# Performance work log

Measured on AMD Instinct MI355X. Metric: run time of the kernel, lower is better.

Reference implementation:

```python
import jax, jax.numpy as jnp
import numpy as np

B, N, R, T, E, H, FE = 2, 512, 64, 128, 64, 8, 4
D = E // H  # head_dim = 8


def _layernorm(x, g, b):
    m = x.mean(-1, keepdims=True)
    v = ((x - m) ** 2).mean(-1, keepdims=True)
    return (x - m) / jnp.sqrt(v + 1e-5) * g + b


def _sattn(v, k, q, Wv, Wk, Wq, Wo, bo, mask):
    # v,k: (Bk,Nk,T,E); q: (Bq,Nq,T,E) with Bq possibly 1 (broadcast on batch)
    Bk, Nk, Tk, _ = v.shape
    Nq = q.shape[1]
    v = v.reshape(Bk, Nk, Tk, H, D) @ Wv
    k = k.reshape(Bk, Nk, Tk, H, D) @ Wk
    q = q.reshape(q.shape[0], Nq, Tk, H, D) @ Wq
    q = jnp.broadcast_to(q, (Bk, Nq, Tk, H, D))
    energy = jnp.einsum('bqthd,bkthd->bqkth', q, k)  # (B,Nq,Nk,T,H)
    if mask is not None:
        m = mask[None, :, :, None, None]
        energy = energy * m + (-1e8) * (1.0 - m)
    # note: non-standard softmax over the QUERY axis (dim=1), after scale+clamp
    att = jax.nn.softmax(jnp.clip(energy * (float(E) ** -0.5), -5.0, 5.0), axis=1)
    out = jnp.einsum('bqkth,bkthd->bqthd', att, v).reshape(Bk, Nq, Tk, E)
    return out @ Wo + bo, att


def setup_inputs() -> dict:
    rng = jax.random.key(0)
    ks = jax.random.split(rng, 40)
    s = 0.05
    inp = {
        'value': jax.random.normal(ks[0], (B, N, T, E), jnp.float32),
        'key': jax.random.normal(ks[1], (B, N, T, E), jnp.float32),
        'query': jax.random.normal(ks[2], (B, N, T, E), jnp.float32),
        'adj_sr': jax.random.randint(ks[3], (N, R), 0, 2).astype(jnp.int32),
        'adj_r': jax.random.randint(ks[4], (R, R), 0, 2).astype(jnp.int32),
        'D_S': jax.random.normal(ks[5], (N, R), jnp.float32) * s,
        'W_emb': jax.random.normal(ks[6], (R, E), jnp.float32) * s,
        'b_emb': jnp.zeros((E,), jnp.float32),
        'I_param': jax.random.normal(ks[7], (R, 1, E), jnp.float32) * s,
        'g1': jnp.ones((E,), jnp.float32), 'beta1': jnp.zeros((E,), jnp.float32),
        'g2': jnp.ones((E,), jnp.float32), 'beta2': jnp.zeros((E,), jnp.float32),
        'W_ff1': jax.random.normal(ks[8], (E, FE * E), jnp.float32) * s,
        'b_ff1': jnp.zeros((FE * E,), jnp.float32),
        'W_ff2': jax.random.normal(ks[9], (FE * E, E), jnp.float32) * s,
        'b_ff2': jnp.zeros((E,), jnp.float32),
        'W_fs': jax.random.normal(ks[10], (E, E), jnp.float32) * s,
        'b_fs': jnp.zeros((E,), jnp.float32),
    }
    i = 11
    for tag in ('sr', 'rr', 'rs'):
        inp['Wv_' + tag] = jax.random.normal(ks[i + 0], (D, D), jnp.float32) * s
        inp['Wk_' + tag] = jax.random.normal(ks[i + 1], (D, D), jnp.float32) * s
        inp['Wq_' + tag] = jax.random.normal(ks[i + 2], (D, D), jnp.float32) * s
        inp['Wo_' + tag] = jax.random.normal(ks[i + 3], (E, E), jnp.float32) * s
        inp['bo_' + tag] = jnp.zeros((E,), jnp.float32)
        i += 4
    return inp


def reference(value, key, query, adj_sr, adj_r, D_S, W_emb, b_emb, I_param,
              g1, beta1, g2, beta2, W_ff1, b_ff1, W_ff2, b_ff2, W_fs, b_fs,
              Wv_sr, Wk_sr, Wq_sr, Wo_sr, bo_sr,
              Wv_rr, Wk_rr, Wq_rr, Wo_rr, bo_rr,
              Wv_rs, Wk_rs, Wq_rs, Wo_rs, bo_rs):
    m_sr = adj_sr.T.astype(jnp.float32)  # (R,N)
    m_r = adj_r.astype(jnp.float32)      # (R,R)
    ds = D_S @ W_emb + b_emb             # (N,E)
    q = query + ds[None, :, None, :]
    k = key + ds[None, :, None, :]
    v = value
    Iq = jnp.broadcast_to(I_param[None], (1, R, T, E))  # I.repeat(1,1,T,1)
    Hh, asr = _sattn(v, k, Iq, Wv_sr, Wk_sr, Wq_sr, Wo_sr, bo_sr, m_sr)
    Hh, arr = _sattn(Hh, Hh, Hh, Wv_rr, Wk_rr, Wq_rr, Wo_rr, bo_rr, m_r)
    attn, ars = _sattn(Hh, Hh, q, Wv_rs, Wk_rs, Wq_rs, Wo_rs, bo_rs, None)
    x = _layernorm(attn + q, g1, beta1)          # dropout=0.0 -> identity
    ff = jax.nn.relu(x @ W_ff1 + b_ff1) @ W_ff2 + b_ff2
    U = _layernorm(ff + x, g2, beta2)
    out = U @ W_fs + b_fs
    return (out, asr, arr, ars, Hh)
```

## Files before the change

### kernel.cpp

```cpp
#include <hip/hip_runtime.h>
#include <hip/hip_bf16.h>

typedef __hip_bfloat16 bf16;

#define Bc 2
#define Nc 512
#define Rc 64
#define Tc 128
#define Ec 64
#define Hc 8
#define THc 1024
#define FFc 256

__device__ __forceinline__ bf16  f2b(float x){ return __float2bfloat16(x); }
__device__ __forceinline__ float us2f(unsigned short u){
  union { unsigned int i; float f; } c; c.i = ((unsigned int)u) << 16; return c.f;
}
__device__ __forceinline__ float clip5(float x){ return fminf(fmaxf(x, -5.0f), 5.0f); }

__device__ __forceinline__ float wave_sum64(float v){
#pragma unroll
  for (int o = 32; o > 0; o >>= 1) v += __shfl_xor(v, o, 64);
  return v;
}
__device__ __forceinline__ void wave_sum64x2(float& a, float& b){
#pragma unroll
  for (int o = 32; o > 0; o >>= 1){
    a += __shfl_xor(a, o, 64);
    b += __shfl_xor(b, o, 64);
  }
}

__device__ __forceinline__ float rowred16_sum(float v){
  v += __shfl_xor(v, 1, 64);
  v += __shfl_xor(v, 2, 64);
  v += __shfl_xor(v, 4, 64);
  v += __shfl_xor(v, 8, 64);
  return v;
}

__global__ __launch_bounds__(64) void k_prep(
    const float* __restrict__ DS, const float* __restrict__ Wemb,
    const float* __restrict__ bemb, const float* __restrict__ Ip,
    const float* __restrict__ Wq, float* __restrict__ ds, float* __restrict__ qhat)
{
  int bid = blockIdx.x, t = threadIdx.x;
  if (bid < Nc){
    int n = bid, e = t;
    __shared__ float row[Rc];
    row[t] = DS[n*Rc + t];
    __syncthreads();
    float acc = bemb[e];
    for (int r = 0; r < Rc; ++r) acc += row[r] * Wemb[r*Ec + e];
    ds[n*Ec + e] = acc;
  } else {
    int r = bid - Nc;
    __shared__ float irow[Ec];
    irow[t] = Ip[r*Ec + t];
    __syncthreads();
    int h = t >> 3, d = t & 7;
    float acc = 0.0f;
#pragma unroll
    for (int d0 = 0; d0 < 8; ++d0) acc += irow[h*8 + d0] * Wq[d0*8 + d];
    qhat[r*Ec + h*8 + d] = acc;
  }
}

__global__ __launch_bounds__(256) void k_proj_sr(
    const float* __restrict__ key, const float* __restrict__ value,
    const float* __restrict__ ds, const float* __restrict__ Wk,
    const float* __restrict__ Wv, float* __restrict__ khat, float* __restrict__ vhat)
{
  __shared__ float wk[64], wv[64];
  int t = threadIdx.x;
  if (t < 64){ wk[t] = Wk[t]; wv[t] = Wv[t]; }
  __syncthreads();
  int u = blockIdx.x*256 + t;
  int h = u & 7;
  int nt = u >> 3;
  int n = (nt / Tc) % Nc;
  const float* kp = key + (size_t)u*8;
  const float* vp = value + (size_t)u*8;
  const float* dsp = ds + n*Ec + h*8;
  float kin[8], vin[8];
#pragma unroll
  for (int d = 0; d < 8; ++d){ kin[d] = kp[d] + dsp[d]; vin[d] = vp[d]; }
  float* ko = khat + (size_t)u*8;
  float* vo = vhat + (size_t)u*8;
#pragma unroll
  for (int d = 0; d < 8; ++d){
    float ka = 0.0f, va = 0.0f;
#pragma unroll
    for (int d0 = 0; d0 < 8; ++d0){ ka += kin[d0]*wk[d0*8+d]; va += vin[d0]*wv[d0*8+d]; }
    ko[d] = ka; vo[d] = va;
  }
}

__global__ __launch_bounds__(256) void k_attn_sr(
    const float* __restrict__ khat, const float* __restrict__ vhat,
    const float* __restrict__ qhat, const int* __restrict__ adj_sr,
    bf16* __restrict__ att_c, float* __restrict__ pre)
{
  __shared__ float accs[4][64][8];
  int bid = blockIdx.x;
  int b = bid >> 10, th = bid & 1023;
  int t = th >> 3, h = th & 7;
  int tid = threadIdx.x;
  int r = tid & 63, w = tid >> 6;
  float q[8];
#pragma unroll
  for (int d = 0; d < 8; ++d) q[d] = qhat[r*Ec + h*8 + d];
  float acc[8] = {0,0,0,0,0,0,0,0};
  int n0 = w*128;
  for (int n = n0; n < n0 + 128; n += 2){
    size_t goA = ((size_t)((b*Nc + n)*Tc + t))*Ec + h*8;
    size_t goB = goA + (size_t)Tc*Ec;
    const float* kA = khat + goA;
    const float* kB = khat + goB;
    float eA = 0.0f, eB = 0.0f;
#pragma unroll
    for (int d = 0; d < 8; ++d){ eA += q[d]*kA[d]; eB += q[d]*kB[d]; }
    int mA = adj_sr[n*Rc + r], mB = adj_sr[(n+1)*Rc + r];
    eA = mA ? clip5(eA*0.125f) : -5.0f;
    eB = mB ? clip5(eB*0.125f) : -5.0f;
    float pA = __expf(eA), pB = __expf(eB);
    float sA = pA, sB = pB;
    wave_sum64x2(sA, sB);
    float aA = pA/sA, aB = pB/sB;
    size_t ao = ((size_t)(b*Nc + n)*THc + th)*Rc + r;
    att_c[ao] = f2b(aA);
    att_c[ao + (size_t)THc*Rc] = f2b(aB);
    const float* vA = vhat + goA;
    const float* vB = vhat + goB;
#pragma unroll
    for (int d = 0; d < 8; ++d) acc[d] += aA*vA[d] + aB*vB[d];
  }
#pragma unroll
  for (int d = 0; d < 8; ++d) accs[w][r][d] = acc[d];
  __syncthreads();
  if (w == 0){
    size_t po = ((size_t)((b*Rc + r)*Tc + t))*Ec + h*8;
#pragma unroll
    for (int d = 0; d < 8; ++d)
      pre[po + d] = accs[0][r][d] + accs[1][r][d] + accs[2][r][d] + accs[3][r][d];
  }
}

__global__ __launch_bounds__(256) void k_attn_rr(
    const float* __restrict__ qh, const float* __restrict__ kh,
    const float* __restrict__ vh, const int* __restrict__ adj_r,
    bf16* __restrict__ att_c, float* __restrict__ pre)
{
  __shared__ float accs[4][64][8];
  int bid = blockIdx.x;
  int b = bid >> 10, th = bid & 1023;
  int t = th >> 3, h = th & 7;
  int tid = threadIdx.x;
  int q = tid & 63, w = tid >> 6;
  size_t qo = ((size_t)((b*Rc + q)*Tc + t))*Ec + h*8;
  float qv[8];
#pragma unroll
  for (int d = 0; d < 8; ++d) qv[d] = qh[qo + d];
  float acc[8] = {0,0,0,0,0,0,0,0};
  int k0 = w*16;
  for (int k = k0; k < k0 + 16; k += 2){
    size_t koA = ((size_t)((b*Rc + k)*Tc + t))*Ec + h*8;
    size_t koB = koA + (size_t)Tc*Ec;
    const float* kA = kh + koA;
    const float* kB = kh + koB;
    float eA = 0.0f, eB = 0.0f;
#pragma unroll
    for (int d = 0; d < 8; ++d){ eA += qv[d]*kA[d]; eB += qv[d]*kB[d]; }
    int mA = adj_r[q*Rc + k], mB = adj_r[q*Rc + k + 1];
    eA = mA ? clip5(eA*0.125f) : -5.0f;
    eB = mB ? clip5(eB*0.125f) : -5.0f;
    float pA = __expf(eA), pB = __expf(eB);
    float sA = pA, sB = pB;
    wave_sum64x2(sA, sB);
    float aA = pA/sA, aB = pB/sB;
    size_t ao = ((size_t)(b*Rc + k)*THc + th)*Rc + q;
    att_c[ao] = f2b(aA);
    att_c[ao + (size_t)THc*Rc] = f2b(aB);
    const float* vA = vh + koA;
    const float* vB = vh + koB;
#pragma unroll
    for (int d = 0; d < 8; ++d) acc[d] += aA*vA[d] + aB*vB[d];
  }
#pragma unroll
  for (int d = 0; d < 8; ++d) accs[w][q][d] = acc[d];
  __syncthreads();
  if (w == 0){
#pragma unroll
    for (int d = 0; d < 8; ++d)
      pre[qo + d] = accs[0][q][d] + accs[1][q][d] + accs[2][q][d] + accs[3][q][d];
  }
}

__global__ __launch_bounds__(512) void k_attn_rs(
    const float* __restrict__ query, const float* __restrict__ ds,
    const float* __restrict__ Wq, const float* __restrict__ kh,
    const float* __restrict__ vh, bf16* __restrict__ att_c, float* __restrict__ pre)
{
  __shared__ float wq[64];
  __shared__ float kl[64][8];
  __shared__ float vl[64][8];
  __shared__ float redS[2][2][8];
  int bid = blockIdx.x;
  int b = bid >> 10, th = bid & 1023;
  int t = th >> 3, h = th & 7;
  int q = threadIdx.x;
  if (q < 64) wq[q] = Wq[q];
  {
    int kk = q >> 3, d = q & 7;
    size_t o = ((size_t)((b*Rc + kk)*Tc + t))*Ec + h*8 + d;
    kl[kk][d] = kh[o];
    vl[kk][d] = vh[o];
  }
  __syncthreads();
  size_t qro = ((size_t)((b*Nc + q)*Tc + t))*Ec + h*8;
  const float* dsp = ds + q*Ec + h*8;
  float xin[8], qv[8];
#pragma unroll
  for (int d = 0; d < 8; ++d) xin[d] = query[qro + d] + dsp[d];
#pragma unroll
  for (int d = 0; d < 8; ++d){
    float a = 0.0f;
#pragma unroll
    for (int d0 = 0; d0 < 8; ++d0) a += xin[d0]*wq[d0*8 + d];
    qv[d] = a;
  }
  float acc[8] = {0,0,0,0,0,0,0,0};
  int lane = q & 63, wv = q >> 6;
  for (int k = 0; k < 64; k += 2){
    float eA = 0.0f, eB = 0.0f;
#pragma unroll
    for (int d = 0; d < 8; ++d){ eA += qv[d]*kl[k][d]; eB += qv[d]*kl[k+1][d]; }
    eA = clip5(eA*0.125f);
    eB = clip5(eB*0.125f);
    float pA = __expf(eA), pB = __expf(eB);
    float sA = pA, sB = pB;
    wave_sum64x2(sA, sB);
    int pb = (k >> 1) & 1;
    if (lane == 0){ redS[pb][0][wv] = sA; redS[pb][1][wv] = sB; }
    __syncthreads();
    float stA = 0.0f, stB = 0.0f;
#pragma unroll
    for (int i = 0; i < 8; ++i){ stA += redS[pb][0][i]; stB += redS[pb][1][i]; }
    float aA = pA/stA, aB = pB/stB;
    size_t ao = ((size_t)(b*Rc + k)*THc + th)*Nc + q;
    att_c[ao] = f2b(aA);
    att_c[ao + (size_t)THc*Nc] = f2b(aB);
#pragma unroll
    for (int d = 0; d < 8; ++d) acc[d] += aA*vl[k][d] + aB*vl[k+1][d];
  }
#pragma unroll
  for (int d = 0; d < 8; ++d) pre[qro + d] = acc[d];
}

__global__ __launch_bounds__(256) void k_transpose(
    const unsigned short* __restrict__ src, float* __restrict__ dst,
    int W, int C)
{
  __shared__ unsigned short tile[64][66];
  int bid = blockIdx.x;
  int nct = C >> 6;
  int ct = bid % nct; bid /= nct;
  int tht = bid & 15; bid >>= 4;
  int w = bid % W; int b = bid / W;
  int tt = threadIdx.x;
  {
    int cs = tt & 63, i0 = tt >> 6;
    const unsigned short* sb = src + ((size_t)(b*W + w)*THc + tht*64)*C + ct*64;
#pragma unroll
    for (int p = 0; p < 16; ++p){
      int i = i0 + p*4;
      tile[i][cs] = sb[(size_t)i*C + cs];
    }
  }
  __syncthreads();
  {
    int i = tt & 63, c0 = tt >> 6;
#pragma unroll
    for (int p = 0; p < 16; ++p){
      int cs = c0 + p*4;
      int c = ct*64 + cs;
      dst[((size_t)(b*C + c)*W + w)*THc + tht*64 + i] = us2f(tile[i][cs]);
    }
  }
}

__global__ __launch_bounds__(256) void k_wo(
    const float* __restrict__ pre, const float* __restrict__ Wo,
    const float* __restrict__ bo, float* __restrict__ outf,
    float* __restrict__ outf2, int nrows)
{
  int gt = blockIdx.x*256 + threadIdx.x;
  int row = gt >> 6, lane = gt & 63;
  if (row >= nrows) return;
  float xin = pre[(size_t)row*64 + lane];
  float acc = bo[lane];
  for (int e = 0; e < 64; ++e){
    float xe = __shfl(xin, e, 64);
    acc += xe * Wo[e*64 + lane];
  }
  outf[(size_t)row*64 + lane] = acc;
  if (outf2) outf2[(size_t)row*64 + lane] = acc;
}

__global__ __launch_bounds__(256) void k_proj3(
    const float* __restrict__ src, const float* Wq, const float* Wk, const float* Wv,
    float* qh, float* kh, float* vh, int nunits)
{
  __shared__ float wq[64], wk[64], wv[64];
  int t = threadIdx.x;
  if (t < 64){
    wq[t] = Wq ? Wq[t] : 0.0f;
    wk[t] = Wk[t];
    wv[t] = Wv[t];
  }
  __syncthreads();
  int u = blockIdx.x*256 + t;
  if (u >= nunits) return;
  const float* sp = src + (size_t)u*8;
  float xin[8];
#pragma unroll
  for (int d = 0; d < 8; ++d) xin[d] = sp[d];
#pragma unroll
  for (int d = 0; d < 8; ++d){
    float qa = 0.0f, ka = 0.0f, va = 0.0f;
#pragma unroll
    for (int d0 = 0; d0 < 8; ++d0){
      qa += xin[d0]*wq[d0*8 + d];
      ka += xin[d0]*wk[d0*8 + d];
      va += xin[d0]*wv[d0*8 + d];
    }
    if (qh) qh[(size_t)u*8 + d] = qa;
    kh[(size_t)u*8 + d] = ka;
    vh[(size_t)u*8 + d] = va;
  }
}

__device__ __forceinline__ void gemm64x64(
    const float (* __restrict__ Xs)[68], const float* __restrict__ W,
    int Wld, int r0, int c0, float acc[4][4])
{
#pragma unroll 4
  for (int k = 0; k < 64; k += 4){
    float4 xr0 = *(const float4*)&Xs[r0+0][k];
    float4 xr1 = *(const float4*)&Xs[r0+1][k];
    float4 xr2 = *(const float4*)&Xs[r0+2][k];
    float4 xr3 = *(const float4*)&Xs[r0+3][k];
#pragma unroll
    for (int kk = 0; kk < 4; ++kk){
      float4 w = *(const float4*)&W[(size_t)(k+kk)*Wld + c0];
      float x0 = (&xr0.x)[kk], x1 = (&xr1.x)[kk];
      float x2 = (&xr2.x)[kk], x3 = (&xr3.x)[kk];
      acc[0][0] += x0*w.x; acc[0][1] += x0*w.y; acc[0][2] += x0*w.z; acc[0][3] += x0*w.w;
      acc[1][0] += x1*w.x; acc[1][1] += x1*w.y; acc[1][2] += x1*w.z; acc[1][3] += x1*w.w;
      acc[2][0] += x2*w.x; acc[2][1] += x2*w.y; acc[2][2] += x2*w.z; acc[2][3] += x2*w.w;
      acc[3][0] += x3*w.x; acc[3][1] += x3*w.y; acc[3][2] += x3*w.z; acc[3][3] += x3*w.w;
    }
  }
}

__device__ __forceinline__ void ln64(
    const float acc[4][4], float4 g, float4 b, float out[4][4])
{
#pragma unroll
  for (int i = 0; i < 4; ++i){
    float s = acc[i][0] + acc[i][1] + acc[i][2] + acc[i][3];
    float m = rowred16_sum(s) * (1.0f/64.0f);
    float d0 = acc[i][0] - m, d1 = acc[i][1] - m, d2 = acc[i][2] - m, d3 = acc[i][3] - m;
    float vv = d0*d0 + d1*d1 + d2*d2 + d3*d3;
    float var = rowred16_sum(vv) * (1.0f/64.0f);
    float rs = rsqrtf(var + 1e-5f);
    out[i][0] = d0*rs*g.x + b.x;
    out[i][1] = d1*rs*g.y + b.y;
    out[i][2] = d2*rs*g.z + b.z;
    out[i][3] = d3*rs*g.w + b.w;
  }
}

__global__ __launch_bounds__(256) void k_tail(
    const float* __restrict__ pre3, const float* __restrict__ query,
    const float* __restrict__ ds,
    const float* __restrict__ Wo, const float* __restrict__ bo,
    const float* __restrict__ g1, const float* __restrict__ be1,
    const float* __restrict__ W1, const float* __restrict__ b1,
    const float* __restrict__ W2, const float* __restrict__ b2,
    const float* __restrict__ g2, const float* __restrict__ be2,
    const float* __restrict__ Wfs, const float* __restrict__ bfs,
    float* __restrict__ outp)
{
  __shared__ float Xs[64][68];
  __shared__ float Hs[64][68];
  int tid = threadIdx.x;
  int cg = tid & 15, rg = tid >> 4;
  int r0 = rg*4, c0 = cg*4;
  int row_base = blockIdx.x * 64;
  int n = (row_base >> 7) & (Nc - 1);

#pragma unroll
  for (int i = 0; i < 4; ++i){
    float4 t = *(const float4*)&pre3[(size_t)(row_base + r0 + i)*64 + c0];
    *(float4*)&Xs[r0+i][c0] = t;
  }

  float4 bo4  = *(const float4*)&bo[c0];
  float4 ds4  = *(const float4*)&ds[n*64 + c0];
  float4 g14  = *(const float4*)&g1[c0];
  float4 be14 = *(const float4*)&be1[c0];
  float4 b24  = *(const float4*)&b2[c0];
  float4 g24  = *(const float4*)&g2[c0];
  float4 be24 = *(const float4*)&be2[c0];
  float4 bfs4 = *(const float4*)&bfs[c0];
  __syncthreads();

  float acc[4][4];
#pragma unroll
  for (int i = 0; i < 4; ++i){
    acc[i][0] = bo4.x; acc[i][1] = bo4.y; acc[i][2] = bo4.z; acc[i][3] = bo4.w;
  }
  gemm64x64(Xs, Wo, 64, r0, c0, acc);
#pragma unroll
  for (int i = 0; i < 4; ++i){
    float4 qv = *(const float4*)&query[(size_t)(row_base + r0 + i)*64 + c0];
    acc[i][0] += qv.x + ds4.x;
    acc[i][1] += qv.y + ds4.y;
    acc[i][2] += qv.z + ds4.z;
    acc[i][3] += qv.w + ds4.w;
  }
  float xt[4][4];
  ln64(acc, g14, be14, xt);
  __syncthreads();
#pragma unroll
  for (int i = 0; i < 4; ++i)
    *(float4*)&Xs[r0+i][c0] = make_float4(xt[i][0], xt[i][1], xt[i][2], xt[i][3]);
  __syncthreads();

  float ff[4][4];
#pragma unroll
  for (int i = 0; i < 4; ++i){
    ff[i][0] = b24.x; ff[i][1] = b24.y; ff[i][2] = b24.z; ff[i][3] = b24.w;
  }
  for (int p = 0; p < 4; ++p){
    float4 b14 = *(const float4*)&b1[p*64 + c0];
    float h[4][4];
#pragma unroll
    for (int i = 0; i < 4; ++i){
      h[i][0] = b14.x; h[i][1] = b14.y; h[i][2] = b14.z; h[i][3] = b14.w;
    }
    gemm64x64(Xs, W1 + p*64, 256, r0, c0, h);
#pragma unroll
    for (int i = 0; i < 4; ++i){
      h[i][0] = fmaxf(h[i][0], 0.0f); h[i][1] = fmaxf(h[i][1], 0.0f);
      h[i][2] = fmaxf(h[i][2], 0.0f); h[i][3] = fmaxf(h[i][3], 0.0f);
    }
    __syncthreads();
#pragma unroll
    for (int i = 0; i < 4; ++i)
      *(float4*)&Hs[r0+i][c0] = make_float4(h[i][0], h[i][1], h[i][2], h[i][3]);
    __syncthreads();
    gemm64x64(Hs, W2 + (size_t)p*64*64, 64, r0, c0, ff);
  }

#pragma unroll
  for (int i = 0; i < 4; ++i){
    float4 xv = *(const float4*)&Xs[r0+i][c0];
    ff[i][0] += xv.x; ff[i][1] += xv.y; ff[i][2] += xv.z; ff[i][3] += xv.w;
  }
  float U[4][4];
  ln64(ff, g24, be24, U);
  __syncthreads();
#pragma unroll
  for (int i = 0; i < 4; ++i)
    *(float4*)&Hs[r0+i][c0] = make_float4(U[i][0], U[i][1], U[i][2], U[i][3]);
  __syncthreads();

  float o[4][4];
#pragma unroll
  for (int i = 0; i < 4; ++i){
    o[i][0] = bfs4.x; o[i][1] = bfs4.y; o[i][2] = bfs4.z; o[i][3] = bfs4.w;
  }
  gemm64x64(Hs, Wfs, 64, r0, c0, o);
#pragma unroll
  for (int i = 0; i < 4; ++i)
    *(float4*)&outp[(size_t)(row_base + r0 + i)*64 + c0] =
        make_float4(o[i][0], o[i][1], o[i][2], o[i][3]);
}

extern "C" void kernel_launch(void* const* d_in, const int* in_sizes, int n_in,
                              void* d_out, int out_size, void* d_ws, size_t ws_size,
                              hipStream_t stream)
{
  const float* value = (const float*)d_in[0];
  const float* key   = (const float*)d_in[1];
  const float* query = (const float*)d_in[2];
  const int*  adj_sr = (const int*)d_in[3];
  const int*  adj_r  = (const int*)d_in[4];
  const float* D_S   = (const float*)d_in[5];
  const float* W_emb = (const float*)d_in[6];
  const float* b_emb = (const float*)d_in[7];
  const float* I_par = (const float*)d_in[8];
  const float* g1    = (const float*)d_in[9];
  const float* be1   = (const float*)d_in[10];
  const float* g2    = (const float*)d_in[11];
  const float* be2   = (const float*)d_in[12];
  const float* W_ff1 = (const float*)d_in[13];
  const float* b_ff1 = (const float*)d_in[14];
  const float* W_ff2 = (const float*)d_in[15];
  const float* b_ff2 = (const float*)d_in[16];
  const float* W_fs  = (const float*)d_in[17];
  const float* b_fs  = (const float*)d_in[18];
  const float* Wv_sr = (const float*)d_in[19];
  const float* Wk_sr = (const float*)d_in[20];
  const float* Wq_sr = (const float*)d_in[21];
  const float* Wo_sr = (const float*)d_in[22];
  const float* bo_sr = (const float*)d_in[23];
  const float* Wv_rr = (const float*)d_in[24];
  const float* Wk_rr = (const float*)d_in[25];
  const float* Wq_rr = (const float*)d_in[26];
  const float* Wo_rr = (const float*)d_in[27];
  const float* bo_rr = (const float*)d_in[28];
  const float* Wv_rs = (const float*)d_in[29];
  const float* Wk_rs = (const float*)d_in[30];
  const float* Wq_rs = (const float*)d_in[31];
  const float* Wo_rs = (const float*)d_in[32];
  const float* bo_rs = (const float*)d_in[33];

  float* outp  = (float*)d_out;
  float* o_out = outp;
  float* o_asr = outp + 8388608;
  float* o_arr = outp + 75497472;
  float* o_ars = outp + 83886080;
  float* o_hh  = outp + 150994944;

  float* wsf = (float*)d_ws;
  float* ws_ds   = wsf;
  float* ws_qsr  = wsf + 32768;
  bf16*  ws_att  = (bf16*)(wsf + 36864);
  float* pool    = wsf + 36864 + 33554432;
  float* ws_ksr  = pool;
  float* ws_vsr  = pool + 8388608;
  float* ws_pre1 = pool + 16777216;
  float* ws_hh1  = pool + 17825792;
  float* ws_qrr  = pool;
  float* ws_krr  = pool + 1048576;
  float* ws_vrr  = pool + 2097152;
  float* ws_pre2 = pool + 3145728;
  float* ws_hh2  = pool + 4194304;
  float* ws_krs  = pool + 5242880;
  float* ws_vrs  = pool + 6291456;
  float* ws_pre3 = pool + 7340032;

  k_prep<<<576, 64, 0, stream>>>(D_S, W_emb, b_emb, I_par, Wq_sr, ws_ds, ws_qsr);
  k_proj_sr<<<4096, 256, 0, stream>>>(key, value, ws_ds, Wk_sr, Wv_sr, ws_ksr, ws_vsr);
  k_attn_sr<<<2048, 256, 0, stream>>>(ws_ksr, ws_vsr, ws_qsr, adj_sr, ws_att, ws_pre1);
  k_transpose<<<16384, 256, 0, stream>>>((const unsigned short*)ws_att, o_asr, 512, 64);
  k_wo<<<4096, 256, 0, stream>>>(ws_pre1, Wo_sr, bo_sr, ws_hh1, (float*)nullptr, 16384);

  k_proj3<<<512, 256, 0, stream>>>(ws_hh1, Wq_rr, Wk_rr, Wv_rr,
                                   ws_qrr, ws_krr, ws_vrr, 131072);
  k_attn_rr<<<2048, 256, 0, stream>>>(ws_qrr, ws_krr, ws_vrr, adj_r, ws_att, ws_pre2);
  k_transpose<<<2048, 256, 0, stream>>>((const unsigned short*)ws_att, o_arr, 64, 64);
  k_wo<<<4096, 256, 0, stream>>>(ws_pre2, Wo_rr, bo_rr, ws_hh2, o_hh, 16384);

  k_proj3<<<512, 256, 0, stream>>>(ws_hh2, (const float*)nullptr, Wk_rs, Wv_rs,
                                   (float*)nullptr, ws_krs, ws_vrs, 131072);
  k_attn_rs<<<2048, 512, 0, stream>>>(query, ws_ds, Wq_rs, ws_krs, ws_vrs,
                                      ws_att, ws_pre3);
  k_transpose<<<16384, 256, 0, stream>>>((const unsigned short*)ws_att, o_ars, 64, 512);

  k_tail<<<2048, 256, 0, stream>>>(ws_pre3, query, ws_ds, Wo_rs, bo_rs,
                                   g1, be1, W_ff1, b_ff1, W_ff2, b_ff2,
                                   g2, be2, W_fs, b_fs, o_out);
}
```

Measured before the change: 848.8 us.

## Process all heads per thread in sr/rr attention and write fp32 attention directly

The sr and rr attention kernels now have each thread handle all 8 heads for one (b,t) with 64-wide register q/acc arrays and vectorized float4 loads. Attention weights are written straight into the final output layout as float4, which removes the bf16 staging buffer and the separate transpose launches. The sr kernel splits N into 4 partial sums that k_wo now adds up. Costs are much higher register pressure, lower occupancy (256 blocks for rr), and a 16-step shared-memory reduction with barriers.

```diff
diff --git a/kernel.cpp b/kernel.cpp
--- a/kernel.cpp
+++ b/kernel.cpp
@@ -99,100 +99,154 @@
 __global__ __launch_bounds__(256) void k_attn_sr(
     const float* __restrict__ khat, const float* __restrict__ vhat,
     const float* __restrict__ qhat, const int* __restrict__ adj_sr,
-    bf16* __restrict__ att_c, float* __restrict__ pre)
-{
-  __shared__ float accs[4][64][8];
+    float* __restrict__ o_asr, float* __restrict__ pre_part)
+{
+  __shared__ float red[2][4][64][4];
   int bid = blockIdx.x;
-  int b = bid >> 10, th = bid & 1023;
-  int t = th >> 3, h = th & 7;
+  int nh = bid & 3; int bt = bid >> 2;
+  int t = bt & (Tc - 1); int b = bt >> 7;
   int tid = threadIdx.x;
   int r = tid & 63, w = tid >> 6;
-  float q[8];
-#pragma unroll
-  for (int d = 0; d < 8; ++d) q[d] = qhat[r*Ec + h*8 + d];
-  float acc[8] = {0,0,0,0,0,0,0,0};
-  int n0 = w*128;
-  for (int n = n0; n < n0 + 128; n += 2){
-    size_t goA = ((size_t)((b*Nc + n)*Tc + t))*Ec + h*8;
-    size_t goB = goA + (size_t)Tc*Ec;
-    const float* kA = khat + goA;
-    const float* kB = khat + goB;
-    float eA = 0.0f, eB = 0.0f;
-#pragma unroll
-    for (int d = 0; d < 8; ++d){ eA += q[d]*kA[d]; eB += q[d]*kB[d]; }
-    int mA = adj_sr[n*Rc + r], mB = adj_sr[(n+1)*Rc + r];
-    eA = mA ? clip5(eA*0.125f) : -5.0f;
-    eB = mB ? clip5(eB*0.125f) : -5.0f;
-    float pA = __expf(eA), pB = __expf(eB);
-    float sA = pA, sB = pB;
-    wave_sum64x2(sA, sB);
-    float aA = pA/sA, aB = pB/sB;
-    size_t ao = ((size_t)(b*Nc + n)*THc + th)*Rc + r;
-    att_c[ao] = f2b(aA);
-    att_c[ao + (size_t)THc*Rc] = f2b(aB);
-    const float* vA = vhat + goA;
-    const float* vB = vhat + goB;
-#pragma unroll
-    for (int d = 0; d < 8; ++d) acc[d] += aA*vA[d] + aB*vB[d];
-  }
-#pragma unroll
-  for (int d = 0; d < 8; ++d) accs[w][r][d] = acc[d];
-  __syncthreads();
-  if (w == 0){
-    size_t po = ((size_t)((b*Rc + r)*Tc + t))*Ec + h*8;
-#pragma unroll
-    for (int d = 0; d < 8; ++d)
-      pre[po + d] = accs[0][r][d] + accs[1][r][d] + accs[2][r][d] + accs[3][r][d];
+  float q[64];
+#pragma unroll
+  for (int i = 0; i < 16; ++i)
+    *(float4*)&q[i*4] = *(const float4*)&qhat[r*64 + i*4];
+  float acc[64];
+#pragma unroll
+  for (int i = 0; i < 64; ++i) acc[i] = 0.0f;
+  int n0 = nh*128 + w*32;
+  for (int n = n0; n < n0 + 32; ++n){
+    size_t ko = ((size_t)((b*Nc + n)*Tc + t))*Ec;
+    const float* kp = khat + ko;
+    const float* vp = vhat + ko;
+    int mflag = adj_sr[n*Rc + r];
+    float p[8], s[8];
+#pragma unroll
+    for (int h = 0; h < 8; ++h){
+      float4 ka = *(const float4*)&kp[h*8];
+      float4 kb = *(const float4*)&kp[h*8 + 4];
+      float e = q[h*8+0]*ka.x + q[h*8+1]*ka.y + q[h*8+2]*ka.z + q[h*8+3]*ka.w
+              + q[h*8+4]*kb.x + q[h*8+5]*kb.y + q[h*8+6]*kb.z + q[h*8+7]*kb.w;
+      e = mflag ? clip5(e*0.125f) : -5.0f;
+      p[h] = __expf(e);
+      s[h] = p[h];
+    }
+#pragma unroll
+    for (int o = 32; o > 0; o >>= 1){
+#pragma unroll
+      for (int h = 0; h < 8; ++h) s[h] += __shfl_xor(s[h], o, 64);
+    }
+    float a[8];
+#pragma unroll
+    for (int h = 0; h < 8; ++h) a[h] = p[h] * __builtin_amdgcn_rcpf(s[h]);
+    size_t ao = ((size_t)((b*Rc + r)*Nc + n))*THc + t*8;
+    *(float4*)&o_asr[ao]     = make_float4(a[0], a[1], a[2], a[3]);
+    *(float4*)&o_asr[ao + 4] = make_float4(a[4], a[5], a[6], a[7]);
+#pragma unroll
+    for (int h = 0; h < 8; ++h){
+      float4 va = *(const float4*)&vp[h*8];
+      float4 vb = *(const float4*)&vp[h*8 + 4];
+      float ah = a[h];
+      acc[h*8+0] += ah*va.x; acc[h*8+1] += ah*va.y;
+      acc[h*8+2] += ah*va.z; acc[h*8+3] += ah*va.w;
+      acc[h*8+4] += ah*vb.x; acc[h*8+5] += ah*vb.y;
+      acc[h*8+6] += ah*vb.z; acc[h*8+7] += ah*vb.w;
+    }
+  }
+#pragma unroll
+  for (int c = 0; c < 16; ++c){
+    int par = c & 1;
+    *(float4*)&red[par][w][r][0] =
+        make_float4(acc[c*4+0], acc[c*4+1], acc[c*4+2], acc[c*4+3]);
+    __syncthreads();
+    if (w == 0){
+      float4 s0 = *(const float4*)&red[par][0][r][0];
+      float4 s1 = *(const float4*)&red[par][1][r][0];
+      float4 s2 = *(const float4*)&red[par][2][r][0];
+      float4 s3 = *(const float4*)&red[par][3][r][0];
+      size_t po = (size_t)nh*1048576 +
+                  ((size_t)((b*Rc + r)*Tc + t))*Ec + c*4;
+      *(float4*)&pre_part[po] = make_float4(s0.x+s1.x+s2.x+s3.x,
+                                            s0.y+s1.y+s2.y+s3.y,
+                                            s0.z+s1.z+s2.z+s3.z,
+                                            s0.w+s1.w+s2.w+s3.w);
+    }
   }
 }
 
 __global__ __launch_bounds__(256) void k_attn_rr(
     const float* __restrict__ qh, const float* __restrict__ kh,
     const float* __restrict__ vh, const int* __restrict__ adj_r,
-    bf16* __restrict__ att_c, float* __restrict__ pre)
-{
-  __shared__ float accs[4][64][8];
+    float* __restrict__ o_arr, float* __restrict__ pre)
+{
+  __shared__ float red[2][4][64][4];
   int bid = blockIdx.x;
-  int b = bid >> 10, th = bid & 1023;
-  int t = th >> 3, h = th & 7;
+  int t = bid & (Tc - 1); int b = bid >> 7;
   int tid = threadIdx.x;
-  int q = tid & 63, w = tid >> 6;
-  size_t qo = ((size_t)((b*Rc + q)*Tc + t))*Ec + h*8;
-  float qv[8];
-#pragma unroll
-  for (int d = 0; d < 8; ++d) qv[d] = qh[qo + d];
-  float acc[8] = {0,0,0,0,0,0,0,0};
+  int qq = tid & 63, w = tid >> 6;
+  size_t row = (size_t)(b*Rc + qq)*Tc + t;
+  float q[64];
+#pragma unroll
+  for (int i = 0; i < 16; ++i)
+    *(float4*)&q[i*4] = *(const float4*)&qh[row*64 + i*4];
+  float acc[64];
+#pragma unroll
+  for (int i = 0; i < 64; ++i) acc[i] = 0.0f;
   int k0 = w*16;
-  for (int k = k0; k < k0 + 16; k += 2){
-    size_t koA = ((size_t)((b*Rc + k)*Tc + t))*Ec + h*8;
-    size_t koB = koA + (size_t)Tc*Ec;
-    const float* kA = kh + koA;
-    const float* kB = kh + koB;
-    float eA = 0.0f, eB = 0.0f;
-#pragma unroll
-    for (int d = 0; d < 8; ++d){ eA += qv[d]*kA[d]; eB += qv[d]*kB[d]; }
-    int mA = adj_r[q*Rc + k], mB = adj_r[q*Rc + k + 1];
-    eA = mA ? clip5(eA*0.125f) : -5.0f;
-    eB = mB ? clip5(eB*0.125f) : -5.0f;
-    float pA = __expf(eA), pB = __expf(eB);
-    float sA = pA, sB = pB;
-    wave_sum64x2(sA, sB);
-    float aA = pA/sA, aB = pB/sB;
-    size_t ao = ((size_t)(b*Rc + k)*THc + th)*Rc + q;
-    att_c[ao] = f2b(aA);
-    att_c[ao + (size_t)THc*Rc] = f2b(aB);
-    const float* vA = vh + koA;
-    const float* vB = vh + koB;
-#pragma unroll
-    for (int d = 0; d < 8; ++d) acc[d] += aA*vA[d] + aB*vB[d];
-  }
-#pragma unroll
-  for (int d = 0; d < 8; ++d) accs[w][q][d] = acc[d];
-  __syncthreads();
-  if (w == 0){
-#pragma unroll
-    for (int d = 0; d < 8; ++d)
-      pre[qo + d] = accs[0][q][d] + accs[1][q][d] + accs[2][q][d] + accs[3][q][d];
+  for (int k = k0; k < k0 + 16; ++k){
+    size_t ko = ((size_t)((b*Rc + k)*Tc + t))*Ec;
+    const float* kp = kh + ko;
+    const float* vp = vh + ko;
+    int mflag = adj_r[qq*Rc + k];
+    float p[8], s[8];
+#pragma unroll
+    for (int h = 0; h < 8; ++h){
+      float4 ka = *(const float4*)&kp[h*8];
+      float4 kb = *(const float4*)&kp[h*8 + 4];
+      float e = q[h*8+0]*ka.x + q[h*8+1]*ka.y + q[h*8+2]*ka.z + q[h*8+3]*ka.w
+              + q[h*8+4]*kb.x + q[h*8+5]*kb.y + q[h*8+6]*kb.z + q[h*8+7]*kb.w;
+      e = mflag ? clip5(e*0.125f) : -5.0f;
+      p[h] = __expf(e);
+      s[h] = p[h];
+    }
+#pragma unroll
+    for (int o = 32; o > 0; o >>= 1){
+#pragma unroll
+      for (int h = 0; h < 8; ++h) s[h] += __shfl_xor(s[h], o, 64);
+    }
+    float a[8];
+#pragma unroll
+    for (int h = 0; h < 8; ++h) a[h] = p[h] * __builtin_amdgcn_rcpf(s[h]);
+    size_t ao = ((size_t)((b*Rc + qq)*Rc + k))*THc + t*8;
+    *(float4*)&o_arr[ao]     = make_float4(a[0], a[1], a[2], a[3]);
+    *(float4*)&o_arr[ao + 4] = make_float4(a[4], a[5], a[6], a[7]);
+#pragma unroll
+    for (int h = 0; h < 8; ++h){
+      float4 va = *(const float4*)&vp[h*8];
+      float4 vb = *(const float4*)&vp[h*8 + 4];
+      float ah = a[h];
+      acc[h*8+0] += ah*va.x; acc[h*8+1] += ah*va.y;
+      acc[h*8+2] += ah*va.z; acc[h*8+3] += ah*va.w;
+      acc[h*8+4] += ah*vb.x; acc[h*8+5] += ah*vb.y;
+      acc[h*8+6] += ah*vb.z; acc[h*8+7] += ah*vb.w;
+    }
+  }
+#pragma unroll
+  for (int c = 0; c < 16; ++c){
+    int par = c & 1;
+    *(float4*)&red[par][w][qq][0] =
+        make_float4(acc[c*4+0], acc[c*4+1], acc[c*4+2], acc[c*4+3]);
+    __syncthreads();
+    if (w == 0){
+      float4 s0 = *(const float4*)&red[par][0][qq][0];
+      float4 s1 = *(const float4*)&red[par][1][qq][0];
+      float4 s2 = *(const float4*)&red[par][2][qq][0];
+      float4 s3 = *(const float4*)&red[par][3][qq][0];
+      *(float4*)&pre[row*64 + c*4] = make_float4(s0.x+s1.x+s2.x+s3.x,
+                                                 s0.y+s1.y+s2.y+s3.y,
+                                                 s0.z+s1.z+s2.z+s3.z,
+                                                 s0.w+s1.w+s2.w+s3.w);
+    }
   }
 }
 
@@ -290,14 +344,17 @@
 }
 
 __global__ __launch_bounds__(256) void k_wo(
-    const float* __restrict__ pre, const float* __restrict__ Wo,
+    const float* __restrict__ pre, int nparts, int pstride,
+    const float* __restrict__ Wo,
     const float* __restrict__ bo, float* __restrict__ outf,
     float* __restrict__ outf2, int nrows)
 {
   int gt = blockIdx.x*256 + threadIdx.x;
   int row = gt >> 6, lane = gt & 63;
   if (row >= nrows) return;
-  float xin = pre[(size_t)row*64 + lane];
+  float xin = 0.0f;
+  for (int p2 = 0; p2 < nparts; ++p2)
+    xin += pre[(size_t)p2*pstride + (size_t)row*64 + lane];
   float acc = bo[lane];
   for (int e = 0; e < 64; ++e){
     float xe = __shfl(xin, e, 64);
@@ -539,11 +596,11 @@
   float* ws_ds   = wsf;
   float* ws_qsr  = wsf + 32768;
   bf16*  ws_att  = (bf16*)(wsf + 36864);
+  float* ws_pre1p = wsf + 36864;
   float* pool    = wsf + 36864 + 33554432;
   float* ws_ksr  = pool;
   float* ws_vsr  = pool + 8388608;
-  float* ws_pre1 = pool + 16777216;
-  float* ws_hh1  = pool + 17825792;
+  float* ws_hh1  = pool + 16777216;
   float* ws_qrr  = pool;
   float* ws_krr  = pool + 1048576;
   float* ws_vrr  = pool + 2097152;
@@ -555,15 +612,14 @@
 
   k_prep<<<576, 64, 0, stream>>>(D_S, W_emb, b_emb, I_par, Wq_sr, ws_ds, ws_qsr);
   k_proj_sr<<<4096, 256, 0, stream>>>(key, value, ws_ds, Wk_sr, Wv_sr, ws_ksr, ws_vsr);
-  k_attn_sr<<<2048, 256, 0, stream>>>(ws_ksr, ws_vsr, ws_qsr, adj_sr, ws_att, ws_pre1);
-  k_transpose<<<16384, 256, 0, stream>>>((const unsigned short*)ws_att, o_asr, 512, 64);
-  k_wo<<<4096, 256, 0, stream>>>(ws_pre1, Wo_sr, bo_sr, ws_hh1, (float*)nullptr, 16384);
+  k_attn_sr<<<1024, 256, 0, stream>>>(ws_ksr, ws_vsr, ws_qsr, adj_sr, o_asr, ws_pre1p);
+  k_wo<<<4096, 256, 0, stream>>>(ws_pre1p, 4, 1048576, Wo_sr, bo_sr,
+                                 ws_hh1, (float*)nullptr, 16384);
 
   k_proj3<<<512, 256, 0, stream>>>(ws_hh1, Wq_rr, Wk_rr, Wv_rr,
                                    ws_qrr, ws_krr, ws_vrr, 131072);
-  k_attn_rr<<<2048, 256, 0, stream>>>(ws_qrr, ws_krr, ws_vrr, adj_r, ws_att, ws_pre2);
-  k_transpose<<<2048, 256, 0, stream>>>((const unsigned short*)ws_att, o_arr, 64, 64);
-  k_wo<<<4096, 256, 0, stream>>>(ws_pre2, Wo_rr, bo_rr, ws_hh2, o_hh, 16384);
+  k_attn_rr<<<256, 256, 0, stream>>>(ws_qrr, ws_krr, ws_vrr, adj_r, o_arr, ws_pre2);
+  k_wo<<<4096, 256, 0, stream>>>(ws_pre2, 1, 0, Wo_rr, bo_rr, ws_hh2, o_hh, 16384);
 
   k_proj3<<<512, 256, 0, stream>>>(ws_hh2, (const float*)nullptr, Wk_rs, Wv_rs,
                                    (float*)nullptr, ws_krs, ws_vrs, 131072);
```

New measurement: 991.0 us. +16.8%, slower.

## Recompute sr attention weights in a dedicated writer kernel instead of bf16 staging plus transpose

Applied to the files above, without the earlier changes.

The sr attention kernel no longer writes bf16 attention weights to a staging buffer that a later transpose kernel converts to the output layout. A new kernel recomputes the energies and softmax denominators from khat and qhat, with the queries held in shared memory, and writes asr directly in the final layout with float4 stores. This drops the intermediate buffer round trip and a large transpose launch, at the cost of computing the energies twice. k_wo also gains an unused multi-part summation option.

```diff
diff --git a/kernel.cpp b/kernel.cpp
--- a/kernel.cpp
+++ b/kernel.cpp
@@ -99,7 +99,7 @@
 __global__ __launch_bounds__(256) void k_attn_sr(
     const float* __restrict__ khat, const float* __restrict__ vhat,
     const float* __restrict__ qhat, const int* __restrict__ adj_sr,
-    bf16* __restrict__ att_c, float* __restrict__ pre)
+    float* __restrict__ pre)
 {
   __shared__ float accs[4][64][8];
   int bid = blockIdx.x;
@@ -127,9 +127,6 @@
     float sA = pA, sB = pB;
     wave_sum64x2(sA, sB);
     float aA = pA/sA, aB = pB/sB;
-    size_t ao = ((size_t)(b*Nc + n)*THc + th)*Rc + r;
-    att_c[ao] = f2b(aA);
-    att_c[ao + (size_t)THc*Rc] = f2b(aB);
     const float* vA = vhat + goA;
     const float* vB = vhat + goB;
 #pragma unroll
@@ -143,6 +140,70 @@
 #pragma unroll
     for (int d = 0; d < 8; ++d)
       pre[po + d] = accs[0][r][d] + accs[1][r][d] + accs[2][r][d] + accs[3][r][d];
+  }
+}
+
+__global__ __launch_bounds__(256) void k_asr_write(
+    const float* __restrict__ khat, const float* __restrict__ qhat,
+    const int* __restrict__ adj_sr, float* __restrict__ o_asr)
+{
+  __shared__ float ql[4096];
+  const float EXPM5 = 0.006737946999085467f;
+  int bid = blockIdx.x;
+  int b = bid >> 8, np = bid & 255;
+  int tid = threadIdx.x;
+  int n = np*2 + (tid >> 7);
+  int t = tid & 127;
+#pragma unroll
+  for (int i = 0; i < 16; ++i) ql[i*256 + tid] = qhat[i*256 + tid];
+  __syncthreads();
+  const float* kp = khat + ((size_t)((b*Nc + n)*Tc + t))*Ec;
+  float kr[64];
+#pragma unroll
+  for (int i = 0; i < 16; ++i) *(float4*)&kr[i*4] = *(const float4*)&kp[i*4];
+
+  float s[8] = {0,0,0,0,0,0,0,0};
+  for (int r = 0; r < 64; ++r){
+    int m = adj_sr[n*Rc + r];
+    if (m){
+      const float* qr = &ql[r*64];
+#pragma unroll
+      for (int h = 0; h < 8; ++h){
+        float4 qa = *(const float4*)&qr[h*8];
+        float4 qb = *(const float4*)&qr[h*8 + 4];
+        float e = qa.x*kr[h*8+0] + qa.y*kr[h*8+1] + qa.z*kr[h*8+2] + qa.w*kr[h*8+3]
+                + qb.x*kr[h*8+4] + qb.y*kr[h*8+5] + qb.z*kr[h*8+6] + qb.w*kr[h*8+7];
+        s[h] += __expf(clip5(e*0.125f));
+      }
+    } else {
+#pragma unroll
+      for (int h = 0; h < 8; ++h) s[h] += EXPM5;
+    }
+  }
+  float rs_[8];
+#pragma unroll
+  for (int h = 0; h < 8; ++h) rs_[h] = __builtin_amdgcn_rcpf(s[h]);
+
+  for (int r = 0; r < 64; ++r){
+    int m = adj_sr[n*Rc + r];
+    float a[8];
+    if (m){
+      const float* qr = &ql[r*64];
+#pragma unroll
+      for (int h = 0; h < 8; ++h){
+        float4 qa = *(const float4*)&qr[h*8];
+        float4 qb = *(const float4*)&qr[h*8 + 4];
+        float e = qa.x*kr[h*8+0] + qa.y*kr[h*8+1] + qa.z*kr[h*8+2] + qa.w*kr[h*8+3]
+                + qb.x*kr[h*8+4] + qb.y*kr[h*8+5] + qb.z*kr[h*8+6] + qb.w*kr[h*8+7];
+        a[h] = __expf(clip5(e*0.125f)) * rs_[h];
+      }
+    } else {
+#pragma unroll
+      for (int h = 0; h < 8; ++h) a[h] = EXPM5 * rs_[h];
+    }
+    size_t ao = ((size_t)((b*Rc + r)*Nc + n))*THc + t*8;
+    *(float4*)&o_asr[ao]     = make_float4(a[0], a[1], a[2], a[3]);
+    *(float4*)&o_asr[ao + 4] = make_float4(a[4], a[5], a[6], a[7]);
   }
 }
 
@@ -290,14 +351,17 @@
 }
 
 __global__ __launch_bounds__(256) void k_wo(
-    const float* __restrict__ pre, const float* __restrict__ Wo,
+    const float* __restrict__ pre, int nparts, int pstride,
+    const float* __restrict__ Wo,
     const float* __restrict__ bo, float* __restrict__ outf,
     float* __restrict__ outf2, int nrows)
 {
   int gt = blockIdx.x*256 + threadIdx.x;
   int row = gt >> 6, lane = gt & 63;
   if (row >= nrows) return;
-  float xin = pre[(size_t)row*64 + lane];
+  float xin = 0.0f;
+  for (int p2 = 0; p2 < nparts; ++p2)
+    xin += pre[(size_t)p2*pstride + (size_t)row*64 + lane];
   float acc = bo[lane];
   for (int e = 0; e < 64; ++e){
     float xe = __shfl(xin, e, 64);
@@ -555,15 +619,16 @@
 
   k_prep<<<576, 64, 0, stream>>>(D_S, W_emb, b_emb, I_par, Wq_sr, ws_ds, ws_qsr);
   k_proj_sr<<<4096, 256, 0, stream>>>(key, value, ws_ds, Wk_sr, Wv_sr, ws_ksr, ws_vsr);
-  k_attn_sr<<<2048, 256, 0, stream>>>(ws_ksr, ws_vsr, ws_qsr, adj_sr, ws_att, ws_pre1);
-  k_transpose<<<16384, 256, 0, stream>>>((const unsigned short*)ws_att, o_asr, 512, 64);
-  k_wo<<<4096, 256, 0, stream>>>(ws_pre1, Wo_sr, bo_sr, ws_hh1, (float*)nullptr, 16384);
+  k_attn_sr<<<2048, 256, 0, stream>>>(ws_ksr, ws_vsr, ws_qsr, adj_sr, ws_pre1);
+  k_asr_write<<<512, 256, 0, stream>>>(ws_ksr, ws_qsr, adj_sr, o_asr);
+  k_wo<<<4096, 256, 0, stream>>>(ws_pre1, 1, 0, Wo_sr, bo_sr,
+                                 ws_hh1, (float*)nullptr, 16384);
 
   k_proj3<<<512, 256, 0, stream>>>(ws_hh1, Wq_rr, Wk_rr, Wv_rr,
                                    ws_qrr, ws_krr, ws_vrr, 131072);
   k_attn_rr<<<2048, 256, 0, stream>>>(ws_qrr, ws_krr, ws_vrr, adj_r, ws_att, ws_pre2);
   k_transpose<<<2048, 256, 0, stream>>>((const unsigned short*)ws_att, o_arr, 64, 64);
-  k_wo<<<4096, 256, 0, stream>>>(ws_pre2, Wo_rr, bo_rr, ws_hh2, o_hh, 16384);
+  k_wo<<<4096, 256, 0, stream>>>(ws_pre2, 1, 0, Wo_rr, bo_rr, ws_hh2, o_hh, 16384);
 
   k_proj3<<<512, 256, 0, stream>>>(ws_hh2, (const float*)nullptr, Wk_rs, Wv_rs,
                                    (float*)nullptr, ws_krs, ws_vrs, 131072);
```

Result: no change. 848.2 us (-0.1%).
